# Optimization experiments

Measured on AMD Instinct MI355X. Metric: run time of the kernel, lower is better.

Reference implementation:

```python
import jax, jax.numpy as jnp
import numpy as np

B, A, F, C = 32, 64, 128, 128


def _mlp(h, W0, b0, W1, b1):
    # LinearLayer stack: Linear(2F->C) + ReLU, Linear(C->C) + ReLU
    h = jax.nn.relu(h @ W0 + b0)
    h = jax.nn.relu(h @ W1 + b1)
    return h


def setup_inputs() -> dict:
    key = jax.random.key(0)
    k0, k1, k2 = jax.random.split(key, 3)
    x = jax.random.normal(k0, (B, A, F), dtype=jnp.float32)
    W0 = jax.random.normal(k1, (2 * F, C), dtype=jnp.float32) * (1.0 / np.sqrt(2 * F))
    b0 = jnp.zeros((C,), dtype=jnp.float32)
    W1 = jax.random.normal(k2, (C, C), dtype=jnp.float32) * (1.0 / np.sqrt(C))
    b1 = jnp.zeros((C,), dtype=jnp.float32)
    return {"x": x, "W0": W0, "b0": b0, "W1": W1, "b1": b1}


def reference(x, W0, b0, W1, b1):
    nb, na, nf = x.shape
    # atom_tile[b,i,j]   = x[b,i]  (first atom of the pair)
    # atom_repeat[b,i,j] = x[b,j]  (second atom of the pair)
    xi = jnp.broadcast_to(x[:, :, None, :], (nb, na, na, nf))
    xj = jnp.broadcast_to(x[:, None, :, :], (nb, na, na, nf))
    # pair_x0 = cat(atom_tile, atom_repeat) = [x_i, x_j]
    p0 = jnp.concatenate([xi, xj], axis=-1).reshape(nb * na * na, 2 * nf)
    # pair_x1 = cat(atom_repeat, atom_tile) = [x_j, x_i]
    p1 = jnp.concatenate([xj, xi], axis=-1).reshape(nb * na * na, 2 * nf)
    h0 = _mlp(p0, W0, b0, W1, b1).reshape(nb, na * na, -1)
    h1 = _mlp(p1, W0, b0, W1, b1).reshape(nb, na * na, -1)
    return h0 + h1
```

## Files before the change

kernel.cpp:

```cpp
#include <hip/hip_runtime.h>
#include <hip/hip_bf16.h>

typedef float    f32x4 __attribute__((ext_vector_type(4)));
typedef _Float16 f16x4 __attribute__((ext_vector_type(4)));
typedef _Float16 f16x8 __attribute__((ext_vector_type(8)));
typedef unsigned int   u32x4 __attribute__((ext_vector_type(4)));

#define NB 32
#define NA 64
#define NF 128
#define NC 128

__global__ __launch_bounds__(256) void prep_kernel(
    const float* __restrict__ x, const float* __restrict__ W0,
    const float* __restrict__ b0, const float* __restrict__ W1,
    _Float16* __restrict__ u, _Float16* __restrict__ v,
    _Float16* __restrict__ w1f)
{
    int blk = blockIdx.x, tid = threadIdx.x;
    if (blk < 256) {
        __shared__ __align__(16) _Float16 w0h[32 * 64 * 8];
        int b = blk >> 3, g = (blk >> 1) & 3, half = blk & 1;

        int lane = tid & 63, wave = tid >> 6;
        int llo = lane & 15, lhi = lane >> 4;

        const float* xrow = x + ((size_t)b * NA + g * 16 + llo) * NF;
        f16x8 xf[4];
        #pragma unroll
        for (int kk = 0; kk < 4; ++kk) {
            f32x4 a0 = *(const f32x4*)(xrow + kk * 32 + lhi * 8);
            f32x4 a1 = *(const f32x4*)(xrow + kk * 32 + lhi * 8 + 4);
            #pragma unroll
            for (int e = 0; e < 4; ++e) {
                xf[kk][e]     = (_Float16)a0[e];
                xf[kk][e + 4] = (_Float16)a1[e];
            }
        }

        #pragma unroll
        for (int p = 0; p < 8; ++p) {
            int sl   = p * 256 + tid;
            int frag = sl >> 6;
            int ln   = sl & 63;
            int kk   = frag >> 3, nfc = frag & 7;
            int k0   = half * 128 + kk * 32 + (ln >> 4) * 8;
            int c    = nfc * 16 + (ln & 15);
            f16x8 o;
            #pragma unroll
            for (int e = 0; e < 8; ++e)
                o[e] = (_Float16)W0[(size_t)(k0 + e) * NC + c];
            *(f16x8*)(w0h + (size_t)sl * 8) = o;
        }
        __syncthreads();

        f32x4 acc[2];
        f32x4 z = {0.f, 0.f, 0.f, 0.f};
        acc[0] = z; acc[1] = z;
        #pragma unroll
        for (int kk = 0; kk < 4; ++kk) {
            #pragma unroll
            for (int t = 0; t < 2; ++t) {
                int nfc = wave * 2 + t;
                f16x8 aw = *(const f16x8*)(w0h +
                    (size_t)((kk * 8 + nfc) * 64 + lane) * 8);
                acc[t] = __builtin_amdgcn_mfma_f32_16x16x32_f16(
                    aw, xf[kk], acc[t], 0, 0, 0);
            }
        }

        _Float16* dst = half ? v : u;
        size_t arow = ((size_t)b * NA + g * 16 + llo) * NC;
        #pragma unroll
        for (int t = 0; t < 2; ++t) {
            int nfc = wave * 2 + t;
            int c0  = nfc * 16 + lhi * 4;
            f16x4 o;
            if (half) {
                f32x4 bb = *(const f32x4*)(b0 + c0);
                #pragma unroll
                for (int e = 0; e < 4; ++e)
                    o[e] = (_Float16)(acc[t][e] + bb[e]);
            } else {
                #pragma unroll
                for (int e = 0; e < 4; ++e)
                    o[e] = (_Float16)acc[t][e];
            }
            *(f16x4*)(dst + arow + c0) = o;
        }
    } else {
        int fl   = (blk - 256) * 256 + tid;
        int lane = fl & 63;
        int frag = fl >> 6;
        int kk = frag >> 3, nf = frag & 7;
        int k0 = kk * 32 + (lane >> 4) * 8;
        int n  = nf * 16 + (lane & 15);
        f16x8 o;
        #pragma unroll
        for (int e = 0; e < 8; ++e)
            o[e] = (_Float16)W1[(size_t)(k0 + e) * NC + n];
        *(f16x8*)(w1f + (size_t)fl * 8) = o;
    }
}

__global__ __launch_bounds__(256, 3) void pair_mlp_kernel(
    const float* __restrict__ b1g, const _Float16* __restrict__ u,
    const _Float16* __restrict__ v, const _Float16* __restrict__ w1f,
    float* __restrict__ out)
{
    __shared__ __align__(16) _Float16 u_s[16 * 128];
    __shared__ __align__(16) _Float16 v_s[16 * 128];
    __shared__ __align__(16) _Float16 w_s[32 * 64 * 8];

    int blk = blockIdx.x;
    int b = blk / 36;
    int t = blk % 36;
    int I = 0;
    while (t >= 8 - I) { t -= 8 - I; ++I; }
    int J = I + t;

    int tid = threadIdx.x;

    {
        int row = tid >> 4;
        int c   = tid & 15;
        int ga  = b * NA + ((row < 8) ? (I * 8 + row) : (J * 8 + (row & 7)));
        int sc  = row * 16 + (c ^ (row & 7));
        ((u32x4*)u_s)[sc] = ((const u32x4*)(u + (size_t)ga * NC))[c];
        ((u32x4*)v_s)[sc] = ((const u32x4*)(v + (size_t)ga * NC))[c];
    }
    #pragma unroll
    for (int p = 0; p < 8; ++p)
        ((u32x4*)w_s)[p * 256 + tid] = ((const u32x4*)w1f)[p * 256 + tid];
    __syncthreads();

    int wave = tid >> 6;
    int lane = tid & 63;
    int llo  = lane & 15;
    int lhi  = lane >> 4;
    int r    = wave * 16 + llo;
    int il   = r >> 3;
    int jl   = r & 7;

    f32x4 acc0[8], acc1[8];
    f32x4 z = {0.f, 0.f, 0.f, 0.f};
    #pragma unroll
    for (int nf = 0; nf < 8; ++nf) { acc0[nf] = z; acc1[nf] = z; }

    const f16x8* us = (const f16x8*)u_s;
    const f16x8* vs = (const f16x8*)v_s;
    const f16x8* wf = (const f16x8*)w_s;

    #pragma unroll
    for (int kk = 0; kk < 4; ++kk) {
        int kc  = kk * 4 + lhi;
        int scI = il * 16 + (kc ^ il);
        int scJ = (8 + jl) * 16 + (kc ^ jl);

        f16x8 uIv = us[scI];
        f16x8 vIv = vs[scI];
        f16x8 uJv = us[scJ];
        f16x8 vJv = vs[scJ];

        f16x8 s0 = uIv + vJv;
        f16x8 s1 = uJv + vIv;
        f16x8 h0, h1;
        #pragma unroll
        for (int e = 0; e < 8; ++e) {
            h0[e] = s0[e] < (_Float16)0 ? (_Float16)0 : s0[e];
            h1[e] = s1[e] < (_Float16)0 ? (_Float16)0 : s1[e];
        }

        #pragma unroll
        for (int nf = 0; nf < 8; ++nf) {
            f16x8 w = wf[(kk * 8 + nf) * 64 + lane];
            acc0[nf] = __builtin_amdgcn_mfma_f32_16x16x32_f16(w, h0, acc0[nf], 0, 0, 0);
            acc1[nf] = __builtin_amdgcn_mfma_f32_16x16x32_f16(w, h1, acc1[nf], 0, 0, 0);
        }
    }

    int Ig = I * 8 + il;
    int Jg = J * 8 + jl;
    float* p1 = out + ((size_t)b * 4096 + Ig * 64 + Jg) * 128 + lhi * 4;
    float* p2 = out + ((size_t)b * 4096 + Jg * 64 + Ig) * 128 + lhi * 4;
    bool mirror = (I != J);
    #pragma unroll
    for (int nf = 0; nf < 8; ++nf) {
        f32x4 bias = *(const f32x4*)(b1g + nf * 16 + lhi * 4);
        f32x4 val;
        #pragma unroll
        for (int e = 0; e < 4; ++e)
            val[e] = fmaxf(acc0[nf][e] + bias[e], 0.f) +
                     fmaxf(acc1[nf][e] + bias[e], 0.f);
        *(f32x4*)(p1 + nf * 16) = val;
        if (mirror)
            *(f32x4*)(p2 + nf * 16) = val;
    }
}

extern "C" void kernel_launch(void* const* d_in, const int* in_sizes, int n_in,
                              void* d_out, int out_size, void* d_ws, size_t ws_size,
                              hipStream_t stream)
{
    (void)in_sizes; (void)n_in; (void)out_size; (void)ws_size;
    const float* x  = (const float*)d_in[0];
    const float* W0 = (const float*)d_in[1];
    const float* b0 = (const float*)d_in[2];
    const float* W1 = (const float*)d_in[3];
    const float* b1 = (const float*)d_in[4];
    float* out = (float*)d_out;

    _Float16* u   = (_Float16*)d_ws;
    _Float16* v   = u + (size_t)NB * NA * NC;
    _Float16* w1f = v + (size_t)NB * NA * NC;

    prep_kernel<<<264, 256, 0, stream>>>(x, W0, b0, W1, u, v, w1f);
    pair_mlp_kernel<<<32 * 36, 256, 0, stream>>>(b1, u, v, w1f, out);
}
```

Measured before the change: 29.90 us.

## Repartition prep kernel so each block handles one 16-column slice of W0

The prep kernel's work split changes. Each block previously converted a whole 128x128 half of W0 into shared memory for 16 atoms. Now each block handles all 64 atoms of a batch against a single 16-column slice of W0, and the launch grows from 264 to 520 blocks. This cuts the per-block W0 load and conversion to an eighth, which shortens the prep kernel's critical path. The cost is that output stores become scalar fp16 writes with stride NC, which are less coalesced than the previous f16x4 stores.

```diff
diff --git a/kernel.cpp b/kernel.cpp
--- a/kernel.cpp
+++ b/kernel.cpp
@@ -18,14 +18,14 @@
     _Float16* __restrict__ w1f)
 {
     int blk = blockIdx.x, tid = threadIdx.x;
-    if (blk < 256) {
-        __shared__ __align__(16) _Float16 w0h[32 * 64 * 8];
-        int b = blk >> 3, g = (blk >> 1) & 3, half = blk & 1;
+    int lane = tid & 63, wave = tid >> 6;
+    int llo = lane & 15, lhi = lane >> 4;
 
-        int lane = tid & 63, wave = tid >> 6;
-        int llo = lane & 15, lhi = lane >> 4;
+    if (blk < 512) {
+        __shared__ __align__(16) _Float16 w0l[4 * 64 * 8];
+        int b = blk >> 4, half = (blk >> 3) & 1, nq = blk & 7;
 
-        const float* xrow = x + ((size_t)b * NA + g * 16 + llo) * NF;
+        const float* xrow = x + ((size_t)b * NA + wave * 16 + llo) * NF;
         f16x8 xf[4];
         #pragma unroll
         for (int kk = 0; kk < 4; ++kk) {
@@ -38,63 +38,40 @@
             }
         }
 
-        #pragma unroll
-        for (int p = 0; p < 8; ++p) {
-            int sl   = p * 256 + tid;
-            int frag = sl >> 6;
-            int ln   = sl & 63;
-            int kk   = frag >> 3, nfc = frag & 7;
-            int k0   = half * 128 + kk * 32 + (ln >> 4) * 8;
-            int c    = nfc * 16 + (ln & 15);
+        {
+            int kk = tid >> 6, ln = tid & 63;
+            int k0 = half * 128 + kk * 32 + (ln >> 4) * 8;
+            int c  = nq * 16 + (ln & 15);
             f16x8 o;
             #pragma unroll
             for (int e = 0; e < 8; ++e)
                 o[e] = (_Float16)W0[(size_t)(k0 + e) * NC + c];
-            *(f16x8*)(w0h + (size_t)sl * 8) = o;
+            *(f16x8*)(w0l + (size_t)tid * 8) = o;
         }
         __syncthreads();
 
-        f32x4 acc[2];
-        f32x4 z = {0.f, 0.f, 0.f, 0.f};
-        acc[0] = z; acc[1] = z;
+        f32x4 acc = {0.f, 0.f, 0.f, 0.f};
         #pragma unroll
         for (int kk = 0; kk < 4; ++kk) {
-            #pragma unroll
-            for (int t = 0; t < 2; ++t) {
-                int nfc = wave * 2 + t;
-                f16x8 aw = *(const f16x8*)(w0h +
-                    (size_t)((kk * 8 + nfc) * 64 + lane) * 8);
-                acc[t] = __builtin_amdgcn_mfma_f32_16x16x32_f16(
-                    aw, xf[kk], acc[t], 0, 0, 0);
-            }
+            f16x8 bw = *(const f16x8*)(w0l + (size_t)((kk * 64 + lane)) * 8);
+            acc = __builtin_amdgcn_mfma_f32_16x16x32_f16(xf[kk], bw, acc, 0, 0, 0);
         }
 
         _Float16* dst = half ? v : u;
-        size_t arow = ((size_t)b * NA + g * 16 + llo) * NC;
+        int c = nq * 16 + llo;
+        float bb = half ? b0[c] : 0.f;
         #pragma unroll
-        for (int t = 0; t < 2; ++t) {
-            int nfc = wave * 2 + t;
-            int c0  = nfc * 16 + lhi * 4;
-            f16x4 o;
-            if (half) {
-                f32x4 bb = *(const f32x4*)(b0 + c0);
-                #pragma unroll
-                for (int e = 0; e < 4; ++e)
-                    o[e] = (_Float16)(acc[t][e] + bb[e]);
-            } else {
-                #pragma unroll
-                for (int e = 0; e < 4; ++e)
-                    o[e] = (_Float16)acc[t][e];
-            }
-            *(f16x4*)(dst + arow + c0) = o;
+        for (int q = 0; q < 4; ++q) {
+            int atom = wave * 16 + lhi * 4 + q;
+            dst[((size_t)b * NA + atom) * NC + c] = (_Float16)(acc[q] + bb);
         }
     } else {
-        int fl   = (blk - 256) * 256 + tid;
-        int lane = fl & 63;
+        int fl   = (blk - 512) * 256 + tid;
+        int ln   = fl & 63;
         int frag = fl >> 6;
         int kk = frag >> 3, nf = frag & 7;
-        int k0 = kk * 32 + (lane >> 4) * 8;
-        int n  = nf * 16 + (lane & 15);
+        int k0 = kk * 32 + (ln >> 4) * 8;
+        int n  = nf * 16 + (ln & 15);
         f16x8 o;
         #pragma unroll
         for (int e = 0; e < 8; ++e)
@@ -214,6 +191,6 @@
     _Float16* v   = u + (size_t)NB * NA * NC;
     _Float16* w1f = v + (size_t)NB * NA * NC;
 
-    prep_kernel<<<264, 256, 0, stream>>>(x, W0, b0, W1, u, v, w1f);
+    prep_kernel<<<520, 256, 0, stream>>>(x, W0, b0, W1, u, v, w1f);
     pair_mlp_kernel<<<32 * 36, 256, 0, stream>>>(b1, u, v, w1f, out);
 }
```

Result: no change. 29.66 us (-0.8%).
